# Optimization experiments

Hardware: AMD Instinct MI355X
Metric: run time of the kernel (lower is better)

Reference implementation:

```python
import jax, jax.numpy as jnp
import numpy as np

D, H, L, N, BINS, V = 256, 8, 4, 512, 64, 20
DFF = 4 * D
DH = D // H
LAMBDA_RG = 10.0
STEPS = 10


def _lin(x, W, b):
    # torch nn.Linear convention: W is [out, in]
    return jnp.einsum('...i,oi->...o', x, W) + b


def _ln(x, g, b, eps=1e-5):
    m = x.mean(-1, keepdims=True)
    v = ((x - m) ** 2).mean(-1, keepdims=True)
    return (x - m) / jnp.sqrt(v + eps) * g + b


def _gelu(x):
    return jax.nn.gelu(x, approximate=False)  # torch nn.GELU default = exact erf


def _pos_encoding():
    pos = jnp.arange(N, dtype=jnp.float32)[:, None]
    div = jnp.exp(jnp.arange(0, D, 2, dtype=jnp.float32) * (-np.log(10000.0) / D))
    pe = jnp.zeros((N, D), jnp.float32)
    pe = pe.at[:, 0::2].set(jnp.sin(pos * div))
    pe = pe.at[:, 1::2].set(jnp.cos(pos * div))
    return pe


def _encoder_layer(x, Wqkv, bqkv, Wo, bo, g1, b1n, W1, b1, W2, b2, g2, b2n):
    # post-norm TransformerEncoderLayer, relu FFN, dropout=0 (eval)
    B, n, _ = x.shape
    qkv = _lin(x, Wqkv, bqkv)
    q, k, v = jnp.split(qkv, 3, axis=-1)
    hd = lambda t: t.reshape(B, n, H, DH).transpose(0, 2, 1, 3)
    q, k, v = hd(q), hd(k), hd(v)
    scores = jnp.einsum('bhqd,bhkd->bhqk', q, k) / jnp.sqrt(jnp.float32(DH))
    attn = jax.nn.softmax(scores, axis=-1)
    o = jnp.einsum('bhqk,bhkd->bhqd', attn, v).transpose(0, 2, 1, 3).reshape(B, n, D)
    x = _ln(x + _lin(o, Wo, bo), g1, b1n)
    ff = _lin(jax.nn.relu(_lin(x, W1, b1)), W2, b2)
    return _ln(x + ff, g2, b2n)


def setup_inputs() -> dict:
    key = jax.random.key(0)
    ks = list(jax.random.split(key, 24))
    it = iter(ks)
    w = lambda shape: jax.random.normal(next(it), shape, jnp.float32) * 0.02
    inp = {
        'tokens': jax.random.randint(next(it), (1, N), 0, V, dtype=jnp.int32),
        'noise': jax.random.normal(next(it), (1, N, 3), jnp.float32),
        'emb': w((V, D)),
        'Wqkv': w((L, 3 * D, D)), 'bqkv': jnp.zeros((L, 3 * D), jnp.float32),
        'Wo': w((L, D, D)), 'bo': jnp.zeros((L, D), jnp.float32),
        'ln1_g': jnp.ones((L, D), jnp.float32), 'ln1_b': jnp.zeros((L, D), jnp.float32),
        'W1': w((L, DFF, D)), 'b1': jnp.zeros((L, DFF), jnp.float32),
        'W2': w((L, D, DFF)), 'b2': jnp.zeros((L, D), jnp.float32),
        'ln2_g': jnp.ones((L, D), jnp.float32), 'ln2_b': jnp.zeros((L, D), jnp.float32),
        'aW1': w((D, D)), 'ab1': jnp.zeros((D,), jnp.float32),
        'aW2': w((1, D)), 'ab2': jnp.zeros((1,), jnp.float32),
        'cW': w((D, D)), 'cb': jnp.zeros((D,), jnp.float32),
        'dW1': w((D, 2 * D)), 'db1': jnp.zeros((D,), jnp.float32),
        'dW2': w((BINS, D)), 'db2': jnp.zeros((BINS,), jnp.float32),
        'tW1': w((D, D)), 'tb1': jnp.zeros((D,), jnp.float32),
        'tW2': w((2, D)), 'tb2': jnp.zeros((2,), jnp.float32),
        'pW': w((3, D)), 'pb': jnp.zeros((3,), jnp.float32),
    }
    return inp


def _forward(tokens, noise, emb, Wqkv, bqkv, Wo, bo, ln1_g, ln1_b, W1, b1, W2, b2,
             ln2_g, ln2_b, aW1, ab1, aW2, ab2, cW, cb, dW1, db1, dW2, db2,
             tW1, tb1, tW2, tb2, pW, pb):
    x = emb[tokens] + _pos_encoding()[None]  # [1,N,D]
    for l in range(L):
        x = _encoder_layer(x, Wqkv[l], bqkv[l], Wo[l], bo[l], ln1_g[l], ln1_b[l],
                           W1[l], b1[l], W2[l], b2[l], ln2_g[l], ln2_b[l])
    # AdaptiveAlphaPredictor
    a = jax.nn.sigmoid(_lin(_gelu(_lin(x, aW1, ab1)), aW2, ab2))
    alpha = (1.2 + a * (3.5 - 1.2))[..., 0]  # [1,N]
    # CSOCKernelAttention: distance power-law * exp-decay kernel
    idx = jnp.arange(N, dtype=jnp.float32)
    r = jnp.abs(idx[:, None] - idx[None, :]) + 1e-4  # [N,N]
    alpha_pair = (alpha[..., :, None] + alpha[..., None, :]) * 0.5  # [1,N,N]
    kernel = r[None] ** (-alpha_pair) * jnp.exp(-r[None] / LAMBDA_RG)
    kernel = kernel / (kernel.sum(-1, keepdims=True) + 1e-8)
    latent = jnp.einsum('bij,bjd->bid', kernel, x)
    # ContactPriorHead
    h = _lin(latent, cW, cb)
    contact = jax.nn.sigmoid(jnp.einsum('bid,bjd->bij', h, h))
    # DistogramHead: expand+concat+MLP (memory-bound O(N^2 d))
    xi = jnp.broadcast_to(latent[:, :, None, :], (1, N, N, D))
    xj = jnp.broadcast_to(latent[:, None, :, :], (1, N, N, D))
    pair = jnp.concatenate([xi, xj], axis=-1)  # [1,N,N,2D]
    disto = _lin(_gelu(_lin(pair, dW1, db1)), dW2, db2)  # [1,N,N,BINS]
    # TorsionGenerator
    t = _lin(_gelu(_lin(latent, tW1, tb1)), tW2, tb2)
    phi = jnp.tanh(t[..., 0]) * np.pi
    psi = jnp.tanh(t[..., 1]) * np.pi
    # DiffusionCoordinateInitializer (STEPS is a small fixed constant)
    target = _lin(latent, pW, pb)  # [1,N,3]
    c = noise
    for step in reversed(range(STEPS)):
        a_t = (step + 1) / STEPS
        c = a_t * c + (1.0 - a_t) * target
    return latent, alpha, contact, disto, phi, psi, c


def reference(tokens, noise, emb, Wqkv, bqkv, Wo, bo, ln1_g, ln1_b, W1, b1, W2, b2,
              ln2_g, ln2_b, aW1, ab1, aW2, ab2, cW, cb, dW1, db1, dW2, db2,
              tW1, tb1, tW2, tb2, pW, pb):
    return _forward(tokens, noise, emb, Wqkv, bqkv, Wo, bo, ln1_g, ln1_b, W1, b1,
                    W2, b2, ln2_g, ln2_b, aW1, ab1, aW2, ab2, cW, cb, dW1, db1,
                    dW2, db2, tW1, tb1, tW2, tb2, pW, pb)
```

## Files before the change

kernel.cpp:

```cpp
#include <hip/hip_runtime.h>
#include <hip/hip_bf16.h>

typedef __attribute__((ext_vector_type(8))) short bf16x8;
typedef __attribute__((ext_vector_type(4))) float f32x4;
typedef unsigned short ushort;

#define OFF_QKV 0
#define OFF_WO  786432
#define OFF_W1  1048576
#define OFF_W2  2097152
#define OFF_AW1 3145728
#define OFF_CW  3211264
#define OFF_DW1 3276800
#define OFF_TW1 3407872
#define WB_TOTAL 3473408

__device__ inline float gelu_f(float x) {
    return 0.5f * x * (1.0f + erff(x * 0.70710678118654752f));
}

__device__ inline ushort f2bfu(float x) {
    __hip_bfloat16 b = __float2bfloat16(x);
    return *reinterpret_cast<ushort*>(&b);
}

__device__ inline uint4 pack_bf8(float4 a, float4 b) {
    uint4 p;
    p.x = f2bfu(a.x) | ((unsigned)f2bfu(a.y) << 16);
    p.y = f2bfu(a.z) | ((unsigned)f2bfu(a.w) << 16);
    p.z = f2bfu(b.x) | ((unsigned)f2bfu(b.y) << 16);
    p.w = f2bfu(b.z) | ((unsigned)f2bfu(b.w) << 16);
    return p;
}

__device__ inline float wave_sum(float v) {
#pragma unroll
    for (int o = 32; o > 0; o >>= 1) v += __shfl_xor(v, o);
    return v;
}
__device__ inline float wave_max(float v) {
#pragma unroll
    for (int o = 32; o > 0; o >>= 1) v = fmaxf(v, __shfl_xor(v, o));
    return v;
}

__global__ void convw_k(const float* __restrict__ Wqkv, const float* __restrict__ Wo,
                        const float* __restrict__ W1, const float* __restrict__ W2,
                        const float* __restrict__ aW1, const float* __restrict__ cW,
                        const float* __restrict__ dW1, const float* __restrict__ tW1,
                        ushort* __restrict__ dst) {
    size_t i = ((size_t)blockIdx.x * 256 + threadIdx.x) * 8;
    if (i >= WB_TOTAL) return;
    const float* src;
    size_t off;
    if (i < OFF_WO)        { src = Wqkv; off = i; }
    else if (i < OFF_W1)   { src = Wo;   off = i - OFF_WO; }
    else if (i < OFF_W2)   { src = W1;   off = i - OFF_W1; }
    else if (i < OFF_AW1)  { src = W2;   off = i - OFF_W2; }
    else if (i < OFF_CW)   { src = aW1;  off = i - OFF_AW1; }
    else if (i < OFF_DW1)  { src = cW;   off = i - OFF_CW; }
    else if (i < OFF_TW1)  { src = dW1;  off = i - OFF_DW1; }
    else                   { src = tW1;  off = i - OFF_TW1; }
    float4 f0 = *(const float4*)&src[off];
    float4 f1 = *(const float4*)&src[off + 4];
    *(uint4*)&dst[i] = pack_bf8(f0, f1);
}

__global__ void embed_k(const int* __restrict__ tokens, const float* __restrict__ emb,
                        float* __restrict__ x, ushort* __restrict__ xb) {
    int n = blockIdx.x, t = threadIdx.x;
    float e = emb[(size_t)tokens[n] * 256 + t];
    int k = t >> 1;
    float div = expf((float)(2 * k) * (-9.210340371976184f / 256.0f));
    float arg = (float)n * div;
    float v = e + ((t & 1) ? cosf(arg) : sinf(arg));
    x[(size_t)n * 256 + t] = v;
    xb[(size_t)n * 256 + t] = f2bfu(v);
}

template <int ACT, int OBF>
__global__ __launch_bounds__(256) void gemm_bf(const ushort* __restrict__ A,
                                               const ushort* __restrict__ Wb,
                                               const float* __restrict__ bias,
                                               float* __restrict__ C,
                                               ushort* __restrict__ Cb,
                                               int Nn, int K, int lda, int ldw, int koff,
                                               size_t woff, size_t boff) {
    __shared__ ushort Al[2][2048];
    __shared__ ushort Wl[2][2048];
    const int t = threadIdx.x;
    const int bm = blockIdx.y * 64, bn = blockIdx.x * 64;
    const int lane = t & 63, wv = t >> 6;
    const int lo = lane & 15, hi = lane >> 4;

    const ushort* aptr = A + (size_t)(bm + lane) * lda + wv * 8;
    const ushort* wptr = Wb + woff + (size_t)(bn + lane) * ldw + koff + wv * 8;

    f32x4 acc0 = {0.f, 0.f, 0.f, 0.f}, acc1 = acc0, acc2 = acc0, acc3 = acc0;
    uint4 a = *(const uint4*)aptr;
    uint4 w = *(const uint4*)wptr;
    const int nsteps = K >> 5;
    for (int s = 0; s < nsteps; ++s) {
        const int buf = s & 1;
        *(uint4*)&Al[buf][t * 8] = a;
        *(uint4*)&Wl[buf][t * 8] = w;
        __syncthreads();
        if (s + 1 < nsteps) {
            a = *(const uint4*)(aptr + (s + 1) * 32);
            w = *(const uint4*)(wptr + (s + 1) * 32);
        }
        bf16x8 af = *(bf16x8*)&Al[buf][(hi * 64 + wv * 16 + lo) * 8];
        bf16x8 b0 = *(bf16x8*)&Wl[buf][(hi * 64 + 0 + lo) * 8];
        bf16x8 b1 = *(bf16x8*)&Wl[buf][(hi * 64 + 16 + lo) * 8];
        bf16x8 b2 = *(bf16x8*)&Wl[buf][(hi * 64 + 32 + lo) * 8];
        bf16x8 b3 = *(bf16x8*)&Wl[buf][(hi * 64 + 48 + lo) * 8];
        acc0 = __builtin_amdgcn_mfma_f32_16x16x32_bf16(af, b0, acc0, 0, 0, 0);
        acc1 = __builtin_amdgcn_mfma_f32_16x16x32_bf16(af, b1, acc1, 0, 0, 0);
        acc2 = __builtin_amdgcn_mfma_f32_16x16x32_bf16(af, b2, acc2, 0, 0, 0);
        acc3 = __builtin_amdgcn_mfma_f32_16x16x32_bf16(af, b3, acc3, 0, 0, 0);
    }

    float bv0 = bias ? bias[boff + bn + 0 + lo] : 0.0f;
    float bv1 = bias ? bias[boff + bn + 16 + lo] : 0.0f;
    float bv2 = bias ? bias[boff + bn + 32 + lo] : 0.0f;
    float bv3 = bias ? bias[boff + bn + 48 + lo] : 0.0f;
#pragma unroll
    for (int r = 0; r < 4; ++r) {
        size_t rw = (size_t)(bm + wv * 16 + hi * 4 + r) * Nn + bn;
        float v0 = acc0[r] + bv0, v1 = acc1[r] + bv1, v2 = acc2[r] + bv2, v3 = acc3[r] + bv3;
        if (ACT == 1) {
            v0 = fmaxf(v0, 0.f); v1 = fmaxf(v1, 0.f); v2 = fmaxf(v2, 0.f); v3 = fmaxf(v3, 0.f);
        }
        if (ACT == 2) {
            v0 = gelu_f(v0); v1 = gelu_f(v1); v2 = gelu_f(v2); v3 = gelu_f(v3);
        }
        if (OBF) {
            Cb[rw + 0 + lo] = f2bfu(v0);
            Cb[rw + 16 + lo] = f2bfu(v1);
            Cb[rw + 32 + lo] = f2bfu(v2);
            Cb[rw + 48 + lo] = f2bfu(v3);
        } else {
            C[rw + 0 + lo] = v0;
            C[rw + 16 + lo] = v1;
            C[rw + 32 + lo] = v2;
            C[rw + 48 + lo] = v3;
        }
    }
}

__global__ __launch_bounds__(256) void ffn2_splitk(const ushort* __restrict__ A,
                                                   const ushort* __restrict__ Wb,
                                                   float* __restrict__ yp,
                                                   size_t woff) {
    __shared__ ushort Al[2][2048];
    __shared__ ushort Wl[2][2048];
    const int t = threadIdx.x;
    const int bm = blockIdx.y * 64, bn = blockIdx.x * 64;
    const int ks = blockIdx.z;
    const int lane = t & 63, wv = t >> 6;
    const int lo = lane & 15, hi = lane >> 4;

    const ushort* aptr = A + (size_t)(bm + lane) * 1024 + ks * 256 + wv * 8;
    const ushort* wptr = Wb + woff + (size_t)(bn + lane) * 1024 + ks * 256 + wv * 8;

    f32x4 acc0 = {0.f, 0.f, 0.f, 0.f}, acc1 = acc0, acc2 = acc0, acc3 = acc0;
    uint4 a = *(const uint4*)aptr;
    uint4 w = *(const uint4*)wptr;
    for (int s = 0; s < 8; ++s) {
        const int buf = s & 1;
        *(uint4*)&Al[buf][t * 8] = a;
        *(uint4*)&Wl[buf][t * 8] = w;
        __syncthreads();
        if (s < 7) {
            a = *(const uint4*)(aptr + (s + 1) * 32);
            w = *(const uint4*)(wptr + (s + 1) * 32);
        }
        bf16x8 af = *(bf16x8*)&Al[buf][(hi * 64 + wv * 16 + lo) * 8];
        bf16x8 b0 = *(bf16x8*)&Wl[buf][(hi * 64 + 0 + lo) * 8];
        bf16x8 b1 = *(bf16x8*)&Wl[buf][(hi * 64 + 16 + lo) * 8];
        bf16x8 b2 = *(bf16x8*)&Wl[buf][(hi * 64 + 32 + lo) * 8];
        bf16x8 b3 = *(bf16x8*)&Wl[buf][(hi * 64 + 48 + lo) * 8];
        acc0 = __builtin_amdgcn_mfma_f32_16x16x32_bf16(af, b0, acc0, 0, 0, 0);
        acc1 = __builtin_amdgcn_mfma_f32_16x16x32_bf16(af, b1, acc1, 0, 0, 0);
        acc2 = __builtin_amdgcn_mfma_f32_16x16x32_bf16(af, b2, acc2, 0, 0, 0);
        acc3 = __builtin_amdgcn_mfma_f32_16x16x32_bf16(af, b3, acc3, 0, 0, 0);
    }

    float* yo = yp + (size_t)ks * 131072;
#pragma unroll
    for (int r = 0; r < 4; ++r) {
        size_t rw = (size_t)(bm + wv * 16 + hi * 4 + r) * 256 + bn;
        yo[rw + 0 + lo] = acc0[r];
        yo[rw + 16 + lo] = acc1[r];
        yo[rw + 32 + lo] = acc2[r];
        yo[rw + 48 + lo] = acc3[r];
    }
}

__global__ void ln_res4_k(float* __restrict__ x, const float* __restrict__ yp,
                          const float* __restrict__ b2, size_t b2off,
                          const float* __restrict__ g, const float* __restrict__ b,
                          size_t goff, ushort* __restrict__ xb) {
    int row = blockIdx.x, t = threadIdx.x;
    __shared__ float red[8];
    size_t idx = (size_t)row * 256 + t;
    float v = x[idx] + ((yp[idx] + yp[idx + 131072]) + (yp[idx + 262144] + yp[idx + 393216]))
            + b2[b2off + t];
    float s = wave_sum(v);
    if ((t & 63) == 0) red[t >> 6] = s;
    __syncthreads();
    float mean = (red[0] + red[1] + red[2] + red[3]) * (1.0f / 256.0f);
    float d = v - mean;
    float s2 = wave_sum(d * d);
    if ((t & 63) == 0) red[4 + (t >> 6)] = s2;
    __syncthreads();
    float var = (red[4] + red[5] + red[6] + red[7]) * (1.0f / 256.0f);
    float res = d * rsqrtf(var + 1e-5f) * g[goff + t] + b[goff + t];
    x[idx] = res;
    xb[idx] = f2bfu(res);
}

__global__ __launch_bounds__(256) void heads_k(const ushort* __restrict__ A,
                                               const ushort* __restrict__ Wb,
                                               const float* __restrict__ cb,
                                               const float* __restrict__ db1,
                                               const float* __restrict__ tb1,
                                               float* __restrict__ hbuf,
                                               float* __restrict__ U,
                                               float* __restrict__ Vv,
                                               float* __restrict__ t1t) {
    size_t woff; int ldw, koff, act; const float* bias; float* C;
    const int z = blockIdx.z;
    if (z == 0)      { woff = OFF_CW;  ldw = 256; koff = 0;   bias = cb;      act = 0; C = hbuf; }
    else if (z == 1) { woff = OFF_DW1; ldw = 512; koff = 0;   bias = db1;     act = 0; C = U; }
    else if (z == 2) { woff = OFF_DW1; ldw = 512; koff = 256; bias = nullptr; act = 0; C = Vv; }
    else             { woff = OFF_TW1; ldw = 256; koff = 0;   bias = tb1;     act = 2; C = t1t; }

    __shared__ ushort Al[2][2048];
    __shared__ ushort Wl[2][2048];
    const int t = threadIdx.x;
    const int bm = blockIdx.y * 64, bn = blockIdx.x * 64;
    const int lane = t & 63, wv = t >> 6;
    const int lo = lane & 15, hi = lane >> 4;

    const ushort* aptr = A + (size_t)(bm + lane) * 256 + wv * 8;
    const ushort* wptr = Wb + woff + (size_t)(bn + lane) * ldw + koff + wv * 8;

    f32x4 acc0 = {0.f, 0.f, 0.f, 0.f}, acc1 = acc0, acc2 = acc0, acc3 = acc0;
    uint4 a = *(const uint4*)aptr;
    uint4 w = *(const uint4*)wptr;
    for (int s = 0; s < 8; ++s) {
        const int buf = s & 1;
        *(uint4*)&Al[buf][t * 8] = a;
        *(uint4*)&Wl[buf][t * 8] = w;
        __syncthreads();
        if (s < 7) {
            a = *(const uint4*)(aptr + (s + 1) * 32);
            w = *(const uint4*)(wptr + (s + 1) * 32);
        }
        bf16x8 af = *(bf16x8*)&Al[buf][(hi * 64 + wv * 16 + lo) * 8];
        bf16x8 b0 = *(bf16x8*)&Wl[buf][(hi * 64 + 0 + lo) * 8];
        bf16x8 b1 = *(bf16x8*)&Wl[buf][(hi * 64 + 16 + lo) * 8];
        bf16x8 b2 = *(bf16x8*)&Wl[buf][(hi * 64 + 32 + lo) * 8];
        bf16x8 b3 = *(bf16x8*)&Wl[buf][(hi * 64 + 48 + lo) * 8];
        acc0 = __builtin_amdgcn_mfma_f32_16x16x32_bf16(af, b0, acc0, 0, 0, 0);
        acc1 = __builtin_amdgcn_mfma_f32_16x16x32_bf16(af, b1, acc1, 0, 0, 0);
        acc2 = __builtin_amdgcn_mfma_f32_16x16x32_bf16(af, b2, acc2, 0, 0, 0);
        acc3 = __builtin_amdgcn_mfma_f32_16x16x32_bf16(af, b3, acc3, 0, 0, 0);
    }

    float bv0 = bias ? bias[bn + 0 + lo] : 0.0f;
    float bv1 = bias ? bias[bn + 16 + lo] : 0.0f;
    float bv2 = bias ? bias[bn + 32 + lo] : 0.0f;
    float bv3 = bias ? bias[bn + 48 + lo] : 0.0f;
#pragma unroll
    for (int r = 0; r < 4; ++r) {
        size_t rw = (size_t)(bm + wv * 16 + hi * 4 + r) * 256 + bn;
        float v0 = acc0[r] + bv0, v1 = acc1[r] + bv1, v2 = acc2[r] + bv2, v3 = acc3[r] + bv3;
        if (act == 2) { v0 = gelu_f(v0); v1 = gelu_f(v1); v2 = gelu_f(v2); v3 = gelu_f(v3); }
        C[rw + 0 + lo] = v0;
        C[rw + 16 + lo] = v1;
        C[rw + 32 + lo] = v2;
        C[rw + 48 + lo] = v3;
    }
}

__global__ __launch_bounds__(256) void attn_k(const float* __restrict__ qkv,
                                              ushort* __restrict__ ob) {
    __shared__ float sc[4][512];
    int t = threadIdx.x;
    int w = t >> 6, lane = t & 63;
    int q = blockIdx.x * 4 + w;
    int h = blockIdx.y;
    const float* qptr = qkv + (size_t)q * 768 + h * 32;
    const float* kbase = qkv + 256 + h * 32;
    const float* vbase = qkv + 512 + h * 32;
    float qv[32];
#pragma unroll
    for (int d = 0; d < 32; d += 4) {
        float4 f = *(const float4*)(qptr + d);
        qv[d] = f.x; qv[d + 1] = f.y; qv[d + 2] = f.z; qv[d + 3] = f.w;
    }
    float mx = -1e30f;
    for (int k = lane; k < 512; k += 64) {
        const float* kp = kbase + (size_t)k * 768;
        float s = 0.0f;
#pragma unroll
        for (int d = 0; d < 32; d += 4) {
            float4 f = *(const float4*)(kp + d);
            s = fmaf(qv[d], f.x, s); s = fmaf(qv[d + 1], f.y, s);
            s = fmaf(qv[d + 2], f.z, s); s = fmaf(qv[d + 3], f.w, s);
        }
        s *= 0.17677669529663687f;
        sc[w][k] = s;
        mx = fmaxf(mx, s);
    }
    mx = wave_max(mx);
    float sum = 0.0f;
    for (int k = lane; k < 512; k += 64) {
        float e = expf(sc[w][k] - mx);
        sc[w][k] = e;
        sum += e;
    }
    sum = wave_sum(sum);
    float inv = 1.0f / sum;
    __syncthreads();
    int d = lane & 31, half = lane >> 5;
    const float* vp = vbase + d;
    const int kb = half * 256;
    float a0 = 0.f, a1 = 0.f, a2 = 0.f, a3 = 0.f;
    float a4 = 0.f, a5 = 0.f, a6 = 0.f, a7 = 0.f;
    for (int k = kb; k < kb + 256; k += 8) {
        float4 p0 = *(const float4*)&sc[w][k];
        float4 p1 = *(const float4*)&sc[w][k + 4];
        a0 = fmaf(p0.x, vp[(size_t)(k + 0) * 768], a0);
        a1 = fmaf(p0.y, vp[(size_t)(k + 1) * 768], a1);
        a2 = fmaf(p0.z, vp[(size_t)(k + 2) * 768], a2);
        a3 = fmaf(p0.w, vp[(size_t)(k + 3) * 768], a3);
        a4 = fmaf(p1.x, vp[(size_t)(k + 4) * 768], a4);
        a5 = fmaf(p1.y, vp[(size_t)(k + 5) * 768], a5);
        a6 = fmaf(p1.z, vp[(size_t)(k + 6) * 768], a6);
        a7 = fmaf(p1.w, vp[(size_t)(k + 7) * 768], a7);
    }
    float accv = ((a0 + a1) + (a2 + a3)) + ((a4 + a5) + (a6 + a7));
    accv += __shfl_down(accv, 32);
    if (lane < 32) ob[(size_t)q * 256 + h * 32 + d] = f2bfu(accv * inv);
}

__global__ void ln_res_k(float* __restrict__ x, const float* __restrict__ y,
                         const float* __restrict__ g, const float* __restrict__ b,
                         size_t goff, ushort* __restrict__ xb) {
    int row = blockIdx.x, t = threadIdx.x;
    __shared__ float red[8];
    float v = x[row * 256 + t] + y[row * 256 + t];
    float s = wave_sum(v);
    if ((t & 63) == 0) red[t >> 6] = s;
    __syncthreads();
    float mean = (red[0] + red[1] + red[2] + red[3]) * (1.0f / 256.0f);
    float d = v - mean;
    float s2 = wave_sum(d * d);
    if ((t & 63) == 0) red[4 + (t >> 6)] = s2;
    __syncthreads();
    float var = (red[4] + red[5] + red[6] + red[7]) * (1.0f / 256.0f);
    float res = d * rsqrtf(var + 1e-5f) * g[goff + t] + b[goff + t];
    x[row * 256 + t] = res;
    xb[row * 256 + t] = f2bfu(res);
}

__global__ void alpha_k(const float* __restrict__ t1, const float* __restrict__ aW2,
                        const float* __restrict__ ab2, float* __restrict__ alphaf,
                        float* __restrict__ out_alpha) {
    int t = threadIdx.x, w = t >> 6, lane = t & 63;
    int n = blockIdx.x * 4 + w;
    const float* r = t1 + (size_t)n * 256;
    float s = 0.0f;
    for (int d = lane; d < 256; d += 64) s = fmaf(r[d], aW2[d], s);
    s = wave_sum(s);
    if (lane == 0) {
        float z = s + ab2[0];
        float a = 1.0f / (1.0f + expf(-z));
        float al = 1.2f + 2.3f * a;
        alphaf[n] = al;
        out_alpha[n] = al;
    }
}

__global__ void csock_k(const float* __restrict__ x, const float* __restrict__ alphaf,
                        float* __restrict__ latent, float* __restrict__ out_latent,
                        ushort* __restrict__ latentb) {
    int i = blockIdx.x, t = threadIdx.x;
    __shared__ float wgt[512];
    __shared__ float red[4];
    float ai = alphaf[i];
    float lsum = 0.0f;
    for (int j = t; j < 512; j += 256) {
        float r = fabsf((float)(i - j)) + 1e-4f;
        float ap = 0.5f * (ai + alphaf[j]);
        float wv = powf(r, -ap) * expf(-r * 0.1f);
        wgt[j] = wv;
        lsum += wv;
    }
    float s = wave_sum(lsum);
    if ((t & 63) == 0) red[t >> 6] = s;
    __syncthreads();
    float S = red[0] + red[1] + red[2] + red[3] + 1e-8f;
    float acc = 0.0f;
    for (int j = 0; j < 512; ++j) acc = fmaf(wgt[j], x[(size_t)j * 256 + t], acc);
    float res = acc / S;
    latent[(size_t)i * 256 + t] = res;
    out_latent[(size_t)i * 256 + t] = res;
    latentb[(size_t)i * 256 + t] = f2bfu(res);
}

__global__ __launch_bounds__(256) void finals_k(const float* __restrict__ h,
                                                const float* __restrict__ t1t,
                                                const float* __restrict__ latentf,
                                                const float* __restrict__ tW2,
                                                const float* __restrict__ tb2,
                                                const float* __restrict__ pW,
                                                const float* __restrict__ pb,
                                                const float* __restrict__ noise,
                                                float* __restrict__ out_contact,
                                                float* __restrict__ phi,
                                                float* __restrict__ psi,
                                                float* __restrict__ outc) {
    const int blk = blockIdx.x;
    const int t = threadIdx.x;
    if (blk < 512) {
        int i = blk;
        __shared__ float hi_s[256];
        hi_s[t] = h[(size_t)i * 256 + t];
        __syncthreads();
        for (int j = t; j < 512; j += 256) {
            const float* hj = h + (size_t)j * 256;
            float s = 0.0f;
#pragma unroll 4
            for (int d = 0; d < 256; d += 4) {
                float4 a = *(const float4*)&hi_s[d];
                float4 b = *(const float4*)&hj[d];
                s = fmaf(a.x, b.x, s); s = fmaf(a.y, b.y, s);
                s = fmaf(a.z, b.z, s); s = fmaf(a.w, b.w, s);
            }
            out_contact[(size_t)i * 512 + j] = 1.0f / (1.0f + expf(-s));
        }
    } else if (blk < 640) {
        int w = t >> 6, lane = t & 63;
        int n = (blk - 512) * 4 + w;
        const float* r = t1t + (size_t)n * 256;
        float s0 = 0.0f, s1 = 0.0f;
        for (int d = lane; d < 256; d += 64) {
            float v = r[d];
            s0 = fmaf(v, tW2[d], s0);
            s1 = fmaf(v, tW2[256 + d], s1);
        }
        s0 = wave_sum(s0);
        s1 = wave_sum(s1);
        if (lane == 0) {
            phi[n] = tanhf(s0 + tb2[0]) * 3.14159265358979323846f;
            psi[n] = tanhf(s1 + tb2[1]) * 3.14159265358979323846f;
        }
    } else {
        int idx = (blk - 640) * 256 + t;
        if (idx >= 512 * 3) return;
        int n = idx / 3, a = idx % 3;
        const float* r = latentf + (size_t)n * 256;
        float s = pb[a];
        for (int d = 0; d < 256; ++d) s = fmaf(r[d], pW[(size_t)a * 256 + d], s);
        float c = noise[idx];
#pragma unroll
        for (int st = 9; st >= 0; --st) {
            float at = (float)(st + 1) * 0.1f;
            c = at * c + (1.0f - at) * s;
        }
        outc[idx] = c;
    }
}

__global__ __launch_bounds__(256) void disto_k(const float* __restrict__ U,
                                               const float* __restrict__ V,
                                               const float* __restrict__ dW2,
                                               const float* __restrict__ db2,
                                               float* __restrict__ out) {
    __shared__ short hsl[32 * 32 * 8];
    __shared__ short w2l[32 * 64 * 8];
    const int t = threadIdx.x;
    const int i = blockIdx.x;
    const int jhalf = blockIdx.y;

    {
        const int brow = t >> 2, dq = t & 3;
#pragma unroll
        for (int c = 0; c < 8; ++c) {
            int dblk = dq * 8 + c;
            int d0 = dblk * 8;
            float4 w0 = *(const float4*)&dW2[(size_t)brow * 256 + d0];
            float4 w1 = *(const float4*)&dW2[(size_t)brow * 256 + d0 + 4];
            *(uint4*)&w2l[(dblk * 64 + brow) * 8] = pack_bf8(w0, w1);
        }
    }

    const int wv = t >> 6, lane = t & 63;
    const int lo = lane & 15, hi = lane >> 4;
    const int jt = wv & 1, bh = wv >> 1;
    float dbv0 = db2[(bh * 2 + 0) * 16 + lo];
    float dbv1 = db2[(bh * 2 + 1) * 16 + lo];

    const int jrow = t & 31, dg = t >> 5;

    for (int p = 0; p < 8; ++p) {
        const int j0 = jhalf * 256 + p * 32;
#pragma unroll
        for (int c = 0; c < 4; ++c) {
            int dblk = dg * 4 + c;
            int d0 = dblk * 8;
            float4 u0 = *(const float4*)&U[(size_t)i * 256 + d0];
            float4 u1 = *(const float4*)&U[(size_t)i * 256 + d0 + 4];
            float4 v0 = *(const float4*)&V[(size_t)(j0 + jrow) * 256 + d0];
            float4 v1 = *(const float4*)&V[(size_t)(j0 + jrow) * 256 + d0 + 4];
            float4 h0, h1;
            h0.x = gelu_f(u0.x + v0.x); h0.y = gelu_f(u0.y + v0.y);
            h0.z = gelu_f(u0.z + v0.z); h0.w = gelu_f(u0.w + v0.w);
            h1.x = gelu_f(u1.x + v1.x); h1.y = gelu_f(u1.y + v1.y);
            h1.z = gelu_f(u1.z + v1.z); h1.w = gelu_f(u1.w + v1.w);
            *(uint4*)&hsl[(dblk * 32 + (jrow ^ dblk)) * 8] = pack_bf8(h0, h1);
        }
        __syncthreads();

        f32x4 acc0 = {0.f, 0.f, 0.f, 0.f}, acc1 = acc0;
#pragma unroll
        for (int kk = 0; kk < 8; ++kk) {
            int db = kk * 4 + hi;
            bf16x8 a = *(bf16x8*)&hsl[(db * 32 + ((jt * 16 + lo) ^ db)) * 8];
            bf16x8 b0 = *(bf16x8*)&w2l[(db * 64 + (bh * 2 + 0) * 16 + lo) * 8];
            bf16x8 b1 = *(bf16x8*)&w2l[(db * 64 + (bh * 2 + 1) * 16 + lo) * 8];
            acc0 = __builtin_amdgcn_mfma_f32_16x16x32_bf16(a, b0, acc0, 0, 0, 0);
            acc1 = __builtin_amdgcn_mfma_f32_16x16x32_bf16(a, b1, acc1, 0, 0, 0);
        }
#pragma unroll
        for (int r = 0; r < 4; ++r) {
            size_t jg = (size_t)i * 512 + j0 + jt * 16 + hi * 4 + r;
            out[jg * 64 + (bh * 2 + 0) * 16 + lo] = acc0[r] + dbv0;
            out[jg * 64 + (bh * 2 + 1) * 16 + lo] = acc1[r] + dbv1;
        }
        __syncthreads();
    }
}

extern "C" void kernel_launch(void* const* d_in, const int* in_sizes, int n_in,
                              void* d_out, int out_size, void* d_ws, size_t ws_size,
                              hipStream_t stream) {
    const int* tokens  = (const int*)d_in[0];
    const float* noise = (const float*)d_in[1];
    const float* emb   = (const float*)d_in[2];
    const float* Wqkv  = (const float*)d_in[3];
    const float* bqkv  = (const float*)d_in[4];
    const float* Wo    = (const float*)d_in[5];
    const float* bo    = (const float*)d_in[6];
    const float* ln1_g = (const float*)d_in[7];
    const float* ln1_b = (const float*)d_in[8];
    const float* W1    = (const float*)d_in[9];
    const float* b1    = (const float*)d_in[10];
    const float* W2    = (const float*)d_in[11];
    const float* b2    = (const float*)d_in[12];
    const float* ln2_g = (const float*)d_in[13];
    const float* ln2_b = (const float*)d_in[14];
    const float* aW1   = (const float*)d_in[15];
    const float* ab1   = (const float*)d_in[16];
    const float* aW2   = (const float*)d_in[17];
    const float* ab2   = (const float*)d_in[18];
    const float* cW    = (const float*)d_in[19];
    const float* cb    = (const float*)d_in[20];
    const float* dW1   = (const float*)d_in[21];
    const float* db1   = (const float*)d_in[22];
    const float* dW2   = (const float*)d_in[23];
    const float* db2   = (const float*)d_in[24];
    const float* tW1   = (const float*)d_in[25];
    const float* tb1   = (const float*)d_in[26];
    const float* tW2   = (const float*)d_in[27];
    const float* tb2   = (const float*)d_in[28];
    const float* pW    = (const float*)d_in[29];
    const float* pb    = (const float*)d_in[30];

    float* out         = (float*)d_out;
    float* out_latent  = out;
    float* out_alpha   = out + 131072;
    float* out_contact = out + 131584;
    float* out_disto   = out + 393728;
    float* out_phi     = out + 17170944;
    float* out_psi     = out + 17171456;
    float* out_c       = out + 17171968;

    float* scratch = out_disto;
    float* x    = scratch;
    float* qkv  = scratch + 131072;
    float* t1t  = scratch + 655360;
    float* y    = scratch + 1179648;
    float* hbuf = scratch + 1310720;
    float* t1a  = scratch + 1441792;
    ushort* wb      = (ushort*)(scratch + 2000000);
    ushort* xb      = (ushort*)(scratch + 3740000);
    ushort* ob      = (ushort*)(scratch + 3810000);
    ushort* ffhb    = (ushort*)(scratch + 3880000);
    ushort* latentb = (ushort*)(scratch + 4150000);
    float* yp   = scratch + 4300000;

    float* latentf = (float*)d_ws;
    float* U       = latentf + 131072;
    float* Vv      = U + 131072;
    float* alphaf  = Vv + 131072;

    convw_k<<<1696, 256, 0, stream>>>(Wqkv, Wo, W1, W2, aW1, cW, dW1, tW1, wb);
    embed_k<<<512, 256, 0, stream>>>(tokens, emb, x, xb);

    for (int l = 0; l < 4; ++l) {
        gemm_bf<0, 0><<<dim3(12, 8), 256, 0, stream>>>(xb, wb, bqkv, qkv, nullptr,
                                                       768, 256, 256, 256, 0,
                                                       OFF_QKV + (size_t)l * 196608, (size_t)l * 768);
        attn_k<<<dim3(128, 8), 256, 0, stream>>>(qkv, ob);
        gemm_bf<0, 0><<<dim3(4, 8), 256, 0, stream>>>(ob, wb, bo, y, nullptr,
                                                      256, 256, 256, 256, 0,
                                                      OFF_WO + (size_t)l * 65536, (size_t)l * 256);
        ln_res_k<<<512, 256, 0, stream>>>(x, y, ln1_g, ln1_b, (size_t)l * 256, xb);
        gemm_bf<1, 1><<<dim3(16, 8), 256, 0, stream>>>(xb, wb, b1, nullptr, ffhb,
                                                       1024, 256, 256, 256, 0,
                                                       OFF_W1 + (size_t)l * 262144, (size_t)l * 1024);
        ffn2_splitk<<<dim3(4, 8, 4), 256, 0, stream>>>(ffhb, wb, yp,
                                                       OFF_W2 + (size_t)l * 262144);
        ln_res4_k<<<512, 256, 0, stream>>>(x, yp, b2, (size_t)l * 256,
                                           ln2_g, ln2_b, (size_t)l * 256, xb);
    }

    gemm_bf<2, 0><<<dim3(4, 8), 256, 0, stream>>>(xb, wb, ab1, t1a, nullptr,
                                                  256, 256, 256, 256, 0, OFF_AW1, 0);
    alpha_k<<<128, 256, 0, stream>>>(t1a, aW2, ab2, alphaf, out_alpha);

    csock_k<<<512, 256, 0, stream>>>(x, alphaf, latentf, out_latent, latentb);

    heads_k<<<dim3(4, 8, 4), 256, 0, stream>>>(latentb, wb, cb, db1, tb1,
                                               hbuf, U, Vv, t1t);

    finals_k<<<646, 256, 0, stream>>>(hbuf, t1t, latentf, tW2, tb2, pW, pb, noise,
                                      out_contact, out_phi, out_psi, out_c);

    disto_k<<<dim3(512, 2), 256, 0, stream>>>(U, Vv, dW2, db2, out_disto);
}
```

Before: 452.1 us.

## Build disto GELU A-fragments in registers and drop LDS staging and barriers

The disto kernel now computes each wave's GELU(U+V) activation tile directly in MFMA A-operand register layout instead of writing it to shared memory and reading it back. The U row is hoisted into registers once per block, and each wave covers 16 j rows against all 64 bins with four accumulators. This removes the per-iteration LDS round trip and two barriers per iteration, and the grid halves to 512 blocks. In exchange, register pressure rises, W2 is staged into LDS once per block for half as many blocks, there is less parallelism across the grid, and V loads become strided per lane rather than coalesced rows.

```diff
diff --git a/kernel.cpp b/kernel.cpp
--- a/kernel.cpp
+++ b/kernel.cpp
@@ -481,11 +481,9 @@
                                                const float* __restrict__ dW2,
                                                const float* __restrict__ db2,
                                                float* __restrict__ out) {
-    __shared__ short hsl[32 * 32 * 8];
     __shared__ short w2l[32 * 64 * 8];
     const int t = threadIdx.x;
     const int i = blockIdx.x;
-    const int jhalf = blockIdx.y;
 
     {
         const int brow = t >> 2, dq = t & 3;
@@ -498,51 +496,54 @@
             *(uint4*)&w2l[(dblk * 64 + brow) * 8] = pack_bf8(w0, w1);
         }
     }
+    __syncthreads();
 
     const int wv = t >> 6, lane = t & 63;
     const int lo = lane & 15, hi = lane >> 4;
-    const int jt = wv & 1, bh = wv >> 1;
-    float dbv0 = db2[(bh * 2 + 0) * 16 + lo];
-    float dbv1 = db2[(bh * 2 + 1) * 16 + lo];
-
-    const int jrow = t & 31, dg = t >> 5;
+
+    float4 uf0[8], uf1[8];
+#pragma unroll
+    for (int kk = 0; kk < 8; ++kk) {
+        uf0[kk] = *(const float4*)&U[(size_t)i * 256 + kk * 32 + hi * 8];
+        uf1[kk] = *(const float4*)&U[(size_t)i * 256 + kk * 32 + hi * 8 + 4];
+    }
+    float dbv[4];
+#pragma unroll
+    for (int nt = 0; nt < 4; ++nt) dbv[nt] = db2[nt * 16 + lo];
 
     for (int p = 0; p < 8; ++p) {
-        const int j0 = jhalf * 256 + p * 32;
-#pragma unroll
-        for (int c = 0; c < 4; ++c) {
-            int dblk = dg * 4 + c;
-            int d0 = dblk * 8;
-            float4 u0 = *(const float4*)&U[(size_t)i * 256 + d0];
-            float4 u1 = *(const float4*)&U[(size_t)i * 256 + d0 + 4];
-            float4 v0 = *(const float4*)&V[(size_t)(j0 + jrow) * 256 + d0];
-            float4 v1 = *(const float4*)&V[(size_t)(j0 + jrow) * 256 + d0 + 4];
+        const int j = p * 64 + wv * 16 + lo;
+        const float* vrow = V + (size_t)j * 256;
+        f32x4 acc0 = {0.f, 0.f, 0.f, 0.f}, acc1 = acc0, acc2 = acc0, acc3 = acc0;
+#pragma unroll
+        for (int kk = 0; kk < 8; ++kk) {
+            float4 v0 = *(const float4*)&vrow[kk * 32 + hi * 8];
+            float4 v1 = *(const float4*)&vrow[kk * 32 + hi * 8 + 4];
             float4 h0, h1;
-            h0.x = gelu_f(u0.x + v0.x); h0.y = gelu_f(u0.y + v0.y);
-            h0.z = gelu_f(u0.z + v0.z); h0.w = gelu_f(u0.w + v0.w);
-            h1.x = gelu_f(u1.x + v1.x); h1.y = gelu_f(u1.y + v1.y);
-            h1.z = gelu_f(u1.z + v1.z); h1.w = gelu_f(u1.w + v1.w);
-            *(uint4*)&hsl[(dblk * 32 + (jrow ^ dblk)) * 8] = pack_bf8(h0, h1);
-        }
-        __syncthreads();
-
-        f32x4 acc0 = {0.f, 0.f, 0.f, 0.f}, acc1 = acc0;
-#pragma unroll
-        for (int kk = 0; kk < 8; ++kk) {
+            h0.x = gelu_f(uf0[kk].x + v0.x); h0.y = gelu_f(uf0[kk].y + v0.y);
+            h0.z = gelu_f(uf0[kk].z + v0.z); h0.w = gelu_f(uf0[kk].w + v0.w);
+            h1.x = gelu_f(uf1[kk].x + v1.x); h1.y = gelu_f(uf1[kk].y + v1.y);
+            h1.z = gelu_f(uf1[kk].z + v1.z); h1.w = gelu_f(uf1[kk].w + v1.w);
+            uint4 ap = pack_bf8(h0, h1);
+            bf16x8 a = *(bf16x8*)&ap;
             int db = kk * 4 + hi;
-            bf16x8 a = *(bf16x8*)&hsl[(db * 32 + ((jt * 16 + lo) ^ db)) * 8];
-            bf16x8 b0 = *(bf16x8*)&w2l[(db * 64 + (bh * 2 + 0) * 16 + lo) * 8];
-            bf16x8 b1 = *(bf16x8*)&w2l[(db * 64 + (bh * 2 + 1) * 16 + lo) * 8];
+            bf16x8 b0 = *(bf16x8*)&w2l[(db * 64 + 0 + lo) * 8];
+            bf16x8 b1 = *(bf16x8*)&w2l[(db * 64 + 16 + lo) * 8];
+            bf16x8 b2 = *(bf16x8*)&w2l[(db * 64 + 32 + lo) * 8];
+            bf16x8 b3 = *(bf16x8*)&w2l[(db * 64 + 48 + lo) * 8];
             acc0 = __builtin_amdgcn_mfma_f32_16x16x32_bf16(a, b0, acc0, 0, 0, 0);
             acc1 = __builtin_amdgcn_mfma_f32_16x16x32_bf16(a, b1, acc1, 0, 0, 0);
+            acc2 = __builtin_amdgcn_mfma_f32_16x16x32_bf16(a, b2, acc2, 0, 0, 0);
+            acc3 = __builtin_amdgcn_mfma_f32_16x16x32_bf16(a, b3, acc3, 0, 0, 0);
         }
 #pragma unroll
         for (int r = 0; r < 4; ++r) {
-            size_t jg = (size_t)i * 512 + j0 + jt * 16 + hi * 4 + r;
-            out[jg * 64 + (bh * 2 + 0) * 16 + lo] = acc0[r] + dbv0;
-            out[jg * 64 + (bh * 2 + 1) * 16 + lo] = acc1[r] + dbv1;
-        }
-        __syncthreads();
+            size_t jg = (size_t)i * 512 + p * 64 + wv * 16 + hi * 4 + r;
+            out[jg * 64 + 0 + lo] = acc0[r] + dbv[0];
+            out[jg * 64 + 16 + lo] = acc1[r] + dbv[1];
+            out[jg * 64 + 32 + lo] = acc2[r] + dbv[2];
+            out[jg * 64 + 48 + lo] = acc3[r] + dbv[3];
+        }
     }
 }
 
@@ -642,5 +643,5 @@
     finals_k<<<646, 256, 0, stream>>>(hbuf, t1t, latentf, tW2, tb2, pW, pb, noise,
                                       out_contact, out_phi, out_psi, out_c);
 
-    disto_k<<<dim3(512, 2), 256, 0, stream>>>(U, Vv, dW2, db2, out_disto);
-}
+    disto_k<<<512, 256, 0, stream>>>(U, Vv, dW2, db2, out_disto);
+}
```

Result: no change. 447.6 us (-1.0%).
